# Optimization experiments

Hardware: AMD Instinct MI355X
Metric: run time of the kernel (lower is better)

## Reference

```python
import jax, jax.numpy as jnp
import numpy as np
from jax import lax

EPS = 1e-5
DN = ('NCHW', 'OIHW', 'NCHW')

def _quant_global(w):
    scale = 1.0 / jnp.maximum(jnp.mean(jnp.abs(w)), EPS)
    u = jnp.clip(jnp.round(w * scale), -1.0, 1.0)
    return u, scale

def _quant_per_channel_dw(w):
    # w: [O, 1, kH, kW]; mean |w| over the kernel taps per output channel
    m = jnp.mean(jnp.abs(w).reshape(w.shape[0], w.shape[1], -1), axis=2, keepdims=True)
    scale = 1.0 / jnp.maximum(m, EPS)[..., None]          # [O,1,1,1]
    u = jnp.clip(jnp.round(w * scale), -1.0, 1.0)
    scale_bcast = jnp.transpose(scale, (1, 0, 2, 3))      # [1,O,1,1] broadcasts over y's channels
    return u, scale_bcast

def _ste(w_real, u):
    # straight-through estimator: forward uses u, grad flows to w_real
    return w_real + lax.stop_gradient(u - w_real)

def setup_inputs() -> dict:
    key = jax.random.key(0)
    k1, k2, k3 = jax.random.split(key, 3)
    x = jax.random.normal(k1, (16, 384, 56, 56), dtype=jnp.float32)
    w_dw = jax.random.normal(k2, (384, 1, 3, 3), dtype=jnp.float32) * 0.1
    w_pw = jax.random.normal(k3, (384, 384, 1, 1), dtype=jnp.float32) * 0.05
    return {"x": x, "w_dw": w_dw, "w_pw": w_pw}

def reference(x, w_dw, w_pw):
    C = x.shape[1]
    # depthwise HardTernaryConv (groups=in_chn, per-channel quant, pad=k//2)
    u_dw, s_dw = _quant_per_channel_dw(w_dw)
    y = lax.conv_general_dilated(x, _ste(w_dw, u_dw), window_strides=(1, 1),
                                 padding=((1, 1), (1, 1)),
                                 dimension_numbers=DN, feature_group_count=C)
    y = y / s_dw
    # pointwise 1x1 HardTernaryConv (global scalar quant scale)
    u_pw, s_pw = _quant_global(w_pw)
    y = lax.conv_general_dilated(y, _ste(w_pw, u_pw), window_strides=(1, 1),
                                 padding=((0, 0), (0, 0)), dimension_numbers=DN)
    y = y / s_pw
    return y
```

## Files before the change

kernel.cpp:

```cpp
#include <hip/hip_runtime.h>
#include <hip/hip_bf16.h>

#define CH 384
#define HH 56
#define WW 56
#define HW (HH*WW)
#define NN 16
#define BN 112
#define BK 64

typedef __attribute__((ext_vector_type(4))) float f32x4;
typedef __attribute__((ext_vector_type(8))) short bf16x8;

__device__ float          g_wdw_eff[CH * 9];
__device__ __hip_bfloat16 g_wpw_u[CH * CH];
__device__ float          g_mx_pw;

__global__ __launch_bounds__(256) void partial_kernel(const float* __restrict__ wpw,
                                                      double* __restrict__ part) {
    const int t = threadIdx.x;
    const int base = blockIdx.x * 1536;
    double s = 0.0;
    #pragma unroll
    for (int k = 0; k < 6; ++k) s += (double)fabsf(wpw[base + t + k * 256]);
    #pragma unroll
    for (int off = 32; off > 0; off >>= 1) s += __shfl_down(s, off, 64);
    __shared__ double sred[4];
    if ((t & 63) == 0) sred[t >> 6] = s;
    __syncthreads();
    if (t == 0) part[blockIdx.x] = ((sred[0] + sred[1]) + sred[2]) + sred[3];
}

__global__ __launch_bounds__(512) void quant_kernel(const float* __restrict__ wdw,
                                                    const float* __restrict__ wpw,
                                                    const double* __restrict__ part) {
    const int t = threadIdx.x;
    __shared__ double pl[96];
    __shared__ float s_scale, s_mx;
    if (t < 96) pl[t] = part[t];
    __syncthreads();
    if (t == 0) {
        double tot = 0.0;
        #pragma unroll
        for (int i = 0; i < 96; ++i) tot += pl[i];
        const float mean = (float)(tot / (double)(CH * CH));
        const float mx   = fmaxf(mean, 1e-5f);
        s_mx = mx;
        s_scale = 1.0f / mx;
    }
    __syncthreads();
    const float scale = s_scale;

    const int base = blockIdx.x * 4096 + t * 8;
    const float4 a = *reinterpret_cast<const float4*>(wpw + base);
    const float4 b = *reinterpret_cast<const float4*>(wpw + base + 4);
    const float vin[8] = {a.x, a.y, a.z, a.w, b.x, b.y, b.z, b.w};
    bf16x8 uo;
    #pragma unroll
    for (int k = 0; k < 8; ++k) {
        float u = rintf(vin[k] * scale);
        u = fminf(1.f, fmaxf(-1.f, u));
        __hip_bfloat16 h = __float2bfloat16(u);
        uo[k] = *reinterpret_cast<short*>(&h);
    }
    *reinterpret_cast<bf16x8*>(g_wpw_u + base) = uo;

    if (blockIdx.x == 0) {
        if (t == 0) g_mx_pw = s_mx;
        if (t < CH) {
            const float* w = wdw + t * 9;
            float asum = 0.f;
            #pragma unroll
            for (int k = 0; k < 9; ++k) asum += fabsf(w[k]);
            const float mxd = fmaxf(asum / 9.0f, 1e-5f);
            const float scd = 1.0f / mxd;
            #pragma unroll
            for (int k = 0; k < 9; ++k) {
                float u = rintf(w[k] * scd);
                u = fminf(1.f, fmaxf(-1.f, u));
                g_wdw_eff[t * 9 + k] = u * mxd;
            }
        }
    }
}

__global__ __launch_bounds__(448, 6) void dw_kernel(const float* __restrict__ x,
                                                    __hip_bfloat16* __restrict__ y) {
    __shared__ __attribute__((aligned(16))) char xs[2][21536];
    __shared__ __attribute__((aligned(16))) __hip_bfloat16 ys[224 * 16];

    const int bid  = blockIdx.x;
    const int orig = (bid & 7) * 96 + (bid >> 3);
    const int nc   = orig >> 1;
    const int half = orig & 1;
    const int n    = nc / 24;
    const int cig  = nc % 24;
    const int ci0  = cig * 16;

    const int wv   = threadIdx.x >> 6;
    const int lane = threadIdx.x & 63;
    const int t    = threadIdx.x;

    const int cil = t / 28;
    const int rm  = t - cil * 28;
    const int row = rm / 7;
    const int wc  = rm - row * 7;
    const int w0  = wc * 8;

    const float* wdp = g_wdw_eff + (ci0 + cil) * 9;
    float wt[9];
    #pragma unroll
    for (int k = 0; k < 9; ++k) wt[k] = wdp[k];

    const float* xg = x + ((size_t)n * CH + ci0) * HW;

#define DSTAGE(B, H0) do {                                                        \
    _Pragma("unroll")                                                             \
    for (int _k = 0; _k < 3; ++_k) {                                              \
        const int _s  = (_k * 7 + wv) * 64 + lane;                   \
        const int _ci = _s / 84;                                                  \
        const int _b  = _s - _ci * 84;                                            \
        const int _rb = _b / 14;                                                  \
        const int _cl = _b - _rb * 14;                                            \
        int _xr = (H0) - 1 + _rb;                                                 \
        _xr = _xr < 0 ? 0 : (_xr > HH - 1 ? HH - 1 : _xr);                        \
        __builtin_amdgcn_global_load_lds(                                         \
            (const __attribute__((address_space(1))) void*)                      \
                (xg + (size_t)_ci * HW + _xr * WW + _cl * 4),                     \
            (__attribute__((address_space(3))) void*)(&xs[(B)][_s * 16]),        \
            16, 0, 0);                                                            \
    }                                                                             \
} while (0)

    DSTAGE(0, half * 28);

    #pragma unroll
    for (int i = 0; i < 7; ++i) {
        const int h0  = (half * 7 + i) * 4;
        const int cur = i & 1;
        if (i < 6) {
            DSTAGE(cur ^ 1, h0 + 4);
            asm volatile("s_waitcnt vmcnt(3)" ::: "memory");
        } else {
            asm volatile("s_waitcnt vmcnt(0)" ::: "memory");
        }
        __builtin_amdgcn_s_barrier();
        __builtin_amdgcn_sched_barrier(0);

        const int h = h0 + row;
        const char* xb = xs[cur] + cil * 1344 + row * 224 + wc * 32;
        float acc[8] = {0.f, 0.f, 0.f, 0.f, 0.f, 0.f, 0.f, 0.f};
        #pragma unroll
        for (int r = 0; r < 3; ++r) {
            const char* rowp = xb + r * 224;
            const f32x4 a = *reinterpret_cast<const f32x4*>(rowp);
            const f32x4 b = *reinterpret_cast<const f32x4*>(rowp + 16);
            const float e0 = (wc > 0) ? *reinterpret_cast<const float*>(rowp - 4) : 0.f;
            const float e1 = (wc < 6) ? *reinterpret_cast<const float*>(rowp + 32) : 0.f;
            const float xv[10] = {e0, a.x, a.y, a.z, a.w, b.x, b.y, b.z, b.w, e1};
            const bool dead = (r == 0 && h == 0) || (r == 2 && h == HH - 1);
            #pragma unroll
            for (int d = 0; d < 3; ++d) {
                const float wv3 = dead ? 0.f : wt[r * 3 + d];
                #pragma unroll
                for (int j = 0; j < 8; ++j) acc[j] += wv3 * xv[j + d];
            }
        }
        #pragma unroll
        for (int j = 0; j < 8; ++j) {
            const int px = row * WW + w0 + j;
            ys[px * 16 + (cil ^ (((px >> 3) & 1) << 3))] = __float2bfloat16(acc[j]);
        }
        asm volatile("s_waitcnt lgkmcnt(0)" ::: "memory");
        __builtin_amdgcn_s_barrier();
        __builtin_amdgcn_sched_barrier(0);

        {
            const int px = t >> 1;
            const int g  = t & 1;
            const int c8 = (g ^ ((px >> 3) & 1)) << 3;
            const bf16x8 v = *reinterpret_cast<const bf16x8*>(&ys[px * 16 + c8]);
            *reinterpret_cast<bf16x8*>(
                y + ((size_t)n * HW + (size_t)h0 * WW + px) * CH + ci0 + g * 8) = v;
        }
    }
#undef DSTAGE
}

#define STAGE(B, KC) do {                                                         \
    const int _k0 = (KC) * BK;                                                    \
    _Pragma("unroll")                                                             \
    for (int _i = 0; _i < 4; ++_i) {                                              \
        const int _sb = wv * 4 + _i;                                              \
        if (_sb < 14) {                                                           \
            const int _s  = _sb * 64 + lane;                                      \
            const int _p  = _s >> 3;                                              \
            const int _c8 = (_s & 7) ^ (_p & 7);                                  \
            __builtin_amdgcn_global_load_lds(                                     \
                (const __attribute__((address_space(1))) void*)                  \
                    (yb + (size_t)_p * CH + _k0 + _c8 * 8),                       \
                (__attribute__((address_space(3))) void*)                        \
                    (&blds[(B)][0] + _sb * 512),                                  \
                16, 0, 0);                                                        \
        }                                                                         \
    }                                                                             \
} while (0)

#define LOADA(dst, KC) {                                                          \
    dst[0][0] = *reinterpret_cast<const bf16x8*>(ap0 + (KC) * 64);                \
    dst[0][1] = *reinterpret_cast<const bf16x8*>(ap0 + (KC) * 64 + 32);           \
    dst[1][0] = *reinterpret_cast<const bf16x8*>(ap1 + (KC) * 64);                \
    dst[1][1] = *reinterpret_cast<const bf16x8*>(ap1 + (KC) * 64 + 32); }

__global__ __launch_bounds__(256) void pw_kernel(const __hip_bfloat16* __restrict__ y,
                                                 float* __restrict__ out) {
    __shared__ __attribute__((aligned(16))) __hip_bfloat16 blds[2][BN * BK];

    const int bid  = blockIdx.x;
    const int orig = (bid & 7) * 168 + (bid >> 3);
    const int n  = orig / 84;
    const int r  = orig % 84;
    const int pt = r / 3;
    const int cb = r % 3;
    const int wv   = threadIdx.x >> 6;
    const int lane = threadIdx.x & 63;
    const int lr   = lane & 15;
    const int lk   = lane >> 4;

    const __hip_bfloat16* yb = y + ((size_t)n * HW + (size_t)pt * BN) * CH;
    const __hip_bfloat16* ap0 = g_wpw_u + (size_t)(cb * 128 + wv * 32 + lr) * CH + 8 * lk;
    const __hip_bfloat16* ap1 = ap0 + (size_t)16 * CH;

    f32x4 acc[2][7];
    #pragma unroll
    for (int i = 0; i < 2; ++i)
        #pragma unroll
        for (int j = 0; j < 7; ++j) acc[i][j] = (f32x4){0.f, 0.f, 0.f, 0.f};

    bf16x8 areg[2][2][2];
    STAGE(0, 0);
    LOADA(areg[0], 0);
    __syncthreads();

    #pragma unroll
    for (int kc = 0; kc < 6; ++kc) {
        const int cur = kc & 1;
        if (kc < 5) { STAGE(cur ^ 1, kc + 1); LOADA(areg[cur ^ 1], kc + 1); }
        #pragma unroll
        for (int kk = 0; kk < 2; ++kk) {
            bf16x8 bfr[7];
            #pragma unroll
            for (int j = 0; j < 7; ++j) {
                const int p  = 16 * j + lr;
                const int c8 = (kk * 4 + lk) ^ (p & 7);
                bfr[j] = *reinterpret_cast<const bf16x8*>(&blds[cur][p * 64 + c8 * 8]);
            }
            #pragma unroll
            for (int i = 0; i < 2; ++i)
                #pragma unroll
                for (int j = 0; j < 7; ++j)
                    acc[i][j] = __builtin_amdgcn_mfma_f32_16x16x32_bf16(
                        areg[cur][i][kk], bfr[j], acc[i][j], 0, 0, 0);
        }
        __syncthreads();
    }

    const float s = g_mx_pw;
    float* ob = out + (size_t)n * CH * HW + (size_t)pt * BN;
    #pragma unroll
    for (int i = 0; i < 2; ++i) {
        const int co0 = cb * 128 + wv * 32 + i * 16 + lk * 4;
        #pragma unroll
        for (int j = 0; j < 7; ++j) {
            const int px = 16 * j + lr;
            #pragma unroll
            for (int rr = 0; rr < 4; ++rr)
                ob[(size_t)(co0 + rr) * HW + px] = acc[i][j][rr] * s;
        }
    }
}

__global__ __launch_bounds__(512) void fused_kernel(const float* __restrict__ x,
                                                    float* __restrict__ out) {
    __shared__ __attribute__((aligned(16))) __hip_bfloat16 ylds[64 * CH];
    const int bid  = blockIdx.x;
    const int orig = (bid & 7) * 112 + (bid >> 3);
    const int n = orig / HH, h = orig % HH;
    const float* xn = x + (size_t)n * CH * HW;

    for (int u = threadIdx.x; u < CH * 7; u += 512) {
        const int ci = u / 7;
        const int wc = u % 7;
        const int w0 = wc * 8;
        const float* xp = xn + (size_t)ci * HW;
        const float* wd = g_wdw_eff + ci * 9;
        float acc[8] = {0.f, 0.f, 0.f, 0.f, 0.f, 0.f, 0.f, 0.f};
        #pragma unroll
        for (int dy = -1; dy <= 1; ++dy) {
            const int hh = h + dy;
            if (hh < 0 || hh >= HH) continue;
            const float* row = xp + hh * WW;
            const float4 va = *reinterpret_cast<const float4*>(row + w0);
            const float4 vb = *reinterpret_cast<const float4*>(row + w0 + 4);
            const float left  = (w0 > 0)      ? row[w0 - 1] : 0.f;
            const float right = (w0 + 8 < WW) ? row[w0 + 8] : 0.f;
            const float xv[10] = {left, va.x, va.y, va.z, va.w,
                                  vb.x, vb.y, vb.z, vb.w, right};
            #pragma unroll
            for (int dx = 0; dx < 3; ++dx) {
                const float wvv = wd[(dy + 1) * 3 + dx];
                #pragma unroll
                for (int j = 0; j < 8; ++j) acc[j] += xv[j + dx] * wvv;
            }
        }
        #pragma unroll
        for (int j = 0; j < 8; ++j)
            ylds[(w0 + j) * CH + (ci ^ ((j ^ wc) << 3))] = __float2bfloat16(acc[j]);
    }
    __syncthreads();

    const int wv   = threadIdx.x >> 6;
    const int lane = threadIdx.x & 63;
    const int lr   = lane & 15;
    const int lk   = lane >> 4;
    f32x4 acc[3][4];
    #pragma unroll
    for (int i = 0; i < 3; ++i)
        #pragma unroll
        for (int j = 0; j < 4; ++j) acc[i][j] = (f32x4){0.f, 0.f, 0.f, 0.f};
    const __hip_bfloat16* abase = g_wpw_u + (size_t)(wv * 16 + lr) * CH + 8 * lk;
    for (int k0 = 0; k0 < CH; k0 += 32) {
        bf16x8 bfr[4];
        #pragma unroll
        for (int j = 0; j < 4; ++j) {
            const int row = 16 * j + lr;
            const int sw  = ((row & 7) ^ ((row >> 3) & 7)) << 3;
            bfr[j] = *reinterpret_cast<const bf16x8*>(&ylds[row * CH + ((k0 + 8 * lk) ^ sw)]);
        }
        #pragma unroll
        for (int i = 0; i < 3; ++i) {
            const bf16x8 afr = *reinterpret_cast<const bf16x8*>(abase + (size_t)(i * 128) * CH + k0);
            #pragma unroll
            for (int j = 0; j < 4; ++j)
                acc[i][j] = __builtin_amdgcn_mfma_f32_16x16x32_bf16(afr, bfr[j], acc[i][j], 0, 0, 0);
        }
    }
    const float s = g_mx_pw;
    float* obase = out + (size_t)n * CH * HW + (size_t)h * WW;
    #pragma unroll
    for (int j = 0; j < 4; ++j) {
        const int pix = 16 * j + lr;
        if (pix >= WW) continue;
        #pragma unroll
        for (int i = 0; i < 3; ++i) {
            const int co0 = (wv + 8 * i) * 16 + lk * 4;
            #pragma unroll
            for (int rr = 0; rr < 4; ++rr)
                obase[(size_t)(co0 + rr) * HW + pix] = acc[i][j][rr] * s;
        }
    }
}

extern "C" void kernel_launch(void* const* d_in, const int* in_sizes, int n_in,
                              void* d_out, int out_size, void* d_ws, size_t ws_size,
                              hipStream_t stream) {
    const float* x    = (const float*)d_in[0];
    const float* w_dw = (const float*)d_in[1];
    const float* w_pw = (const float*)d_in[2];
    float* out = (float*)d_out;

    const size_t y_bytes    = (size_t)NN * HW * CH * sizeof(__hip_bfloat16);
    const size_t part_bytes = 96 * sizeof(double);

    if (ws_size >= y_bytes + part_bytes) {
        double* part = (double*)((char*)d_ws + y_bytes);
        partial_kernel<<<96, 256, 0, stream>>>(w_pw, part);
        quant_kernel<<<36, 512, 0, stream>>>(w_dw, w_pw, part);
        __hip_bfloat16* yg = (__hip_bfloat16*)d_ws;
        dw_kernel<<<768, 448, 0, stream>>>(x, yg);
        pw_kernel<<<NN * 28 * 3, 256, 0, stream>>>(yg, out);
    } else if (ws_size >= part_bytes) {
        double* part = (double*)d_ws;
        partial_kernel<<<96, 256, 0, stream>>>(w_pw, part);
        quant_kernel<<<36, 512, 0, stream>>>(w_dw, w_pw, part);
        fused_kernel<<<NN * HH, 512, 0, stream>>>(x, out);
    }
}
```

Measured before the change: 74.99 us.

## Use rolling 12-row LDS ring buffer in depthwise kernel to avoid halo reloads

Replaces the double-buffered 6-row tiles (which reloaded the two halo rows each step) with a 12-row circular LDS buffer, so each step loads only the 4 new input rows. The thread mapping changes so channel is the fastest-varying index, and the ys staging uses a padded pitch of 18 instead of an XOR swizzle. Occupancy is lowered from 6 to 4 blocks per SM and the wait counts now differ per wave. This adds index arithmetic and may bring LDS bank conflicts from the unaligned row pitch and the 4-byte ys reads.

```diff
diff --git a/kernel.cpp b/kernel.cpp
--- a/kernel.cpp
+++ b/kernel.cpp
@@ -9,8 +9,12 @@
 #define BN 112
 #define BK 64
 
+#define XR_STRIDE 3840
+#define YS_PITCH 18
+
 typedef __attribute__((ext_vector_type(4))) float f32x4;
 typedef __attribute__((ext_vector_type(8))) short bf16x8;
+typedef __attribute__((ext_vector_type(4))) unsigned int u32x4;
 
 __device__ float          g_wdw_eff[CH * 9];
 __device__ __hip_bfloat16 g_wpw_u[CH * CH];
@@ -84,10 +88,10 @@
     }
 }
 
-__global__ __launch_bounds__(448, 6) void dw_kernel(const float* __restrict__ x,
+__global__ __launch_bounds__(448, 4) void dw_kernel(const float* __restrict__ x,
                                                     __hip_bfloat16* __restrict__ y) {
-    __shared__ __attribute__((aligned(16))) char xs[2][21536];
-    __shared__ __attribute__((aligned(16))) __hip_bfloat16 ys[224 * 16];
+    __shared__ __attribute__((aligned(16))) char xs[12 * XR_STRIDE];
+    __shared__ __attribute__((aligned(16))) __hip_bfloat16 ys[224 * YS_PITCH];
 
     const int bid  = blockIdx.x;
     const int orig = (bid & 7) * 96 + (bid >> 3);
@@ -97,94 +101,131 @@
     const int cig  = nc % 24;
     const int ci0  = cig * 16;
 
-    const int wv   = threadIdx.x >> 6;
-    const int lane = threadIdx.x & 63;
     const int t    = threadIdx.x;
-
-    const int cil = t / 28;
-    const int rm  = t - cil * 28;
-    const int row = rm / 7;
-    const int wc  = rm - row * 7;
+    const int wv   = t >> 6;
+    const int lane = t & 63;
+
+    const int cil = t & 15;
+    const int rw  = t >> 4;
+    const int row = rw / 7;
+    const int wc  = rw % 7;
     const int w0  = wc * 8;
 
-    const float* wdp = g_wdw_eff + (ci0 + cil) * 9;
+    const float* xg = x + ((size_t)n * CH + ci0) * HW;
+
     float wt[9];
-    #pragma unroll
-    for (int k = 0; k < 9; ++k) wt[k] = wdp[k];
-
-    const float* xg = x + ((size_t)n * CH + ci0) * HW;
-
-#define DSTAGE(B, H0) do {                                                        \
-    _Pragma("unroll")                                                             \
-    for (int _k = 0; _k < 3; ++_k) {                                              \
-        const int _s  = (_k * 7 + wv) * 64 + lane;                   \
-        const int _ci = _s / 84;                                                  \
-        const int _b  = _s - _ci * 84;                                            \
-        const int _rb = _b / 14;                                                  \
-        const int _cl = _b - _rb * 14;                                            \
-        int _xr = (H0) - 1 + _rb;                                                 \
-        _xr = _xr < 0 ? 0 : (_xr > HH - 1 ? HH - 1 : _xr);                        \
-        __builtin_amdgcn_global_load_lds(                                         \
-            (const __attribute__((address_space(1))) void*)                      \
-                (xg + (size_t)_ci * HW + _xr * WW + _cl * 4),                     \
-            (__attribute__((address_space(3))) void*)(&xs[(B)][_s * 16]),        \
-            16, 0, 0);                                                            \
-    }                                                                             \
-} while (0)
-
-    DSTAGE(0, half * 28);
+    {
+        const float* wdp = g_wdw_eff + (ci0 + cil) * 9;
+        #pragma unroll
+        for (int k = 0; k < 9; ++k) wt[k] = wdp[k];
+    }
+
+    const int hbase = half * 28;
+
+    #pragma unroll
+    for (int kk = 0; kk < 4; ++kk) {
+        const int q = wv + 7 * kk;
+        if (q < 24) {
+            const int ro  = q >> 2;
+            const int sub = q & 3;
+            const int R   = hbase - 1 + ro;
+            const int rr  = (R + 12) % 12;
+            const int Rc  = R < 0 ? 0 : (R > HH - 1 ? HH - 1 : R);
+            const int s   = sub * 64 + lane;
+            const int sci = s / 15;
+            const int scl = s - sci * 15;
+            if (s < 240 && scl < 14) {
+                __builtin_amdgcn_global_load_lds(
+                    (const __attribute__((address_space(1))) void*)
+                        (xg + (size_t)sci * HW + Rc * WW + scl * 4),
+                    (__attribute__((address_space(3))) void*)
+                        (xs + rr * XR_STRIDE + sub * 1024),
+                    16, 0, 0);
+            }
+        }
+    }
 
     #pragma unroll
     for (int i = 0; i < 7; ++i) {
-        const int h0  = (half * 7 + i) * 4;
-        const int cur = i & 1;
+        const int h0 = hbase + i * 4;
+
         if (i < 6) {
-            DSTAGE(cur ^ 1, h0 + 4);
-            asm volatile("s_waitcnt vmcnt(3)" ::: "memory");
+            const int RB = h0 + 5;
+            #pragma unroll
+            for (int kk = 0; kk < 3; ++kk) {
+                const int q = wv + 7 * kk;
+                if (q < 16) {
+                    const int ro  = q >> 2;
+                    const int sub = q & 3;
+                    const int R   = RB + ro;
+                    const int rr  = R % 12;
+                    const int Rc  = R > HH - 1 ? HH - 1 : R;
+                    const int s   = sub * 64 + lane;
+                    const int sci = s / 15;
+                    const int scl = s - sci * 15;
+                    if (s < 240 && scl < 14) {
+                        __builtin_amdgcn_global_load_lds(
+                            (const __attribute__((address_space(1))) void*)
+                                (xg + (size_t)sci * HW + Rc * WW + scl * 4),
+                            (__attribute__((address_space(3))) void*)
+                                (xs + rr * XR_STRIDE + sub * 1024),
+                            16, 0, 0);
+                    }
+                }
+            }
+            if (wv < 2) asm volatile("s_waitcnt vmcnt(3)" ::: "memory");
+            else        asm volatile("s_waitcnt vmcnt(2)" ::: "memory");
         } else {
             asm volatile("s_waitcnt vmcnt(0)" ::: "memory");
         }
         __builtin_amdgcn_s_barrier();
         __builtin_amdgcn_sched_barrier(0);
 
-        const int h = h0 + row;
-        const char* xb = xs[cur] + cil * 1344 + row * 224 + wc * 32;
+        const int h   = h0 + row;
+        const int rrb = (h0 + 11) % 12;
+
         float acc[8] = {0.f, 0.f, 0.f, 0.f, 0.f, 0.f, 0.f, 0.f};
         #pragma unroll
         for (int r = 0; r < 3; ++r) {
-            const char* rowp = xb + r * 224;
-            const f32x4 a = *reinterpret_cast<const f32x4*>(rowp);
-            const f32x4 b = *reinterpret_cast<const f32x4*>(rowp + 16);
+            int rr = rrb + row + r; if (rr >= 12) rr -= 12;
+            const char* rowp = xs + rr * XR_STRIDE + (cil * 15 + 2 * wc) * 16;
+            const f32x4 f0 = *reinterpret_cast<const f32x4*>(rowp);
+            const f32x4 f1 = *reinterpret_cast<const f32x4*>(rowp + 16);
             const float e0 = (wc > 0) ? *reinterpret_cast<const float*>(rowp - 4) : 0.f;
-            const float e1 = (wc < 6) ? *reinterpret_cast<const float*>(rowp + 32) : 0.f;
-            const float xv[10] = {e0, a.x, a.y, a.z, a.w, b.x, b.y, b.z, b.w, e1};
+            const float f8 = *reinterpret_cast<const float*>(rowp + 32);
+            const float x9 = (wc < 6) ? f8 : 0.f;
+            const float xv[10] = {e0, f0.x, f0.y, f0.z, f0.w,
+                                  f1.x, f1.y, f1.z, f1.w, x9};
             const bool dead = (r == 0 && h == 0) || (r == 2 && h == HH - 1);
             #pragma unroll
             for (int d = 0; d < 3; ++d) {
-                const float wv3 = dead ? 0.f : wt[r * 3 + d];
+                const float w3 = dead ? 0.f : wt[r * 3 + d];
                 #pragma unroll
-                for (int j = 0; j < 8; ++j) acc[j] += wv3 * xv[j + d];
-            }
-        }
-        #pragma unroll
-        for (int j = 0; j < 8; ++j) {
-            const int px = row * WW + w0 + j;
-            ys[px * 16 + (cil ^ (((px >> 3) & 1) << 3))] = __float2bfloat16(acc[j]);
-        }
+                for (int j = 0; j < 8; ++j) acc[j] += w3 * xv[j + d];
+            }
+        }
+
+        const int pxb = row * WW + w0;
+        #pragma unroll
+        for (int j = 0; j < 8; ++j)
+            ys[(pxb + j) * YS_PITCH + cil] = __float2bfloat16(acc[j]);
+
         asm volatile("s_waitcnt lgkmcnt(0)" ::: "memory");
         __builtin_amdgcn_s_barrier();
         __builtin_amdgcn_sched_barrier(0);
 
         {
-            const int px = t >> 1;
-            const int g  = t & 1;
-            const int c8 = (g ^ ((px >> 3) & 1)) << 3;
-            const bf16x8 v = *reinterpret_cast<const bf16x8*>(&ys[px * 16 + c8]);
-            *reinterpret_cast<bf16x8*>(
-                y + ((size_t)n * HW + (size_t)h0 * WW + px) * CH + ci0 + g * 8) = v;
-        }
-    }
-#undef DSTAGE
+            const int px  = t >> 1;
+            const int oct = t & 1;
+            const unsigned* yp =
+                reinterpret_cast<const unsigned*>(ys + px * YS_PITCH + oct * 8);
+            u32x4 v;
+            v.x = yp[0]; v.y = yp[1]; v.z = yp[2]; v.w = yp[3];
+            *reinterpret_cast<u32x4*>(
+                y + ((size_t)n * HW + (size_t)h0 * WW + px) * CH + ci0 + oct * 8) = v;
+        }
+        __builtin_amdgcn_sched_barrier(0);
+    }
 }
 
 #define STAGE(B, KC) do {                                                         \
```

Result: faster. 65.02 us (-13.3%).
